# Kernel optimization log

Hardware: AMD Instinct MI355X
Metric: run time of the kernel (lower is better)

The kernel has to match this reference:

```python
import jax, jax.numpy as jnp
import numpy as np

B, T, E, H = 8, 1024, 128, 8
S = E // H  # 16, narrow per-head dim


def setup_inputs() -> dict:
    key = jax.random.key(0)
    ks = jax.random.split(key, 7)
    return {
        "x": jax.random.normal(ks[0], (B, T, E), dtype=jnp.float32),
        "masks": jax.random.randint(ks[1], (B, T), 0, 2, dtype=jnp.int32),
        "Wq": jax.random.normal(ks[2], (S, S), dtype=jnp.float32) * 0.05,
        "Wk": jax.random.normal(ks[3], (S, S), dtype=jnp.float32) * 0.05,
        "Wv": jax.random.normal(ks[4], (S, S), dtype=jnp.float32) * 0.05,
        "Wu": jax.random.normal(ks[5], (E, E), dtype=jnp.float32) * 0.05,
        "bu": jnp.zeros((E,), dtype=jnp.float32),
        "temporal_only": 1,
    }


def reference(x, masks, Wq, Wk, Wv, Wu, bu, temporal_only):
    b, t, e = x.shape
    h = H
    s = e // h
    x4 = x.reshape(b, t, h, s)
    # nn.Linear(s, s, bias=False): y = x @ W.T, applied per head
    q = jnp.einsum('bths,ds->bthd', x4, Wq)
    k = jnp.einsum('bths,ds->bthd', x4, Wk)
    v = jnp.einsum('bths,ds->bthd', x4, Wv)
    scale = jnp.float32(e) ** 0.25
    q = q / scale
    k = k / scale
    # (b, h, t, t) attention logits
    dot = jnp.einsum('bqhd,bkhd->bhqk', q, k)
    # temporal_only masking: masks is (b, t), applied on key axis then query axis
    m = masks.astype(bool)
    neg = jnp.float32(-1e9)
    dot = jnp.where(m[:, None, None, :], dot, neg)
    dot = jnp.where(m[:, None, :, None], dot, neg)
    attn = jax.nn.softmax(dot, axis=-1)
    # post-softmax zeroing with the same masks
    attn = jnp.where(m[:, None, None, :], attn, jnp.float32(0.0))
    attn = jnp.where(m[:, None, :, None], attn, jnp.float32(0.0))
    out = jnp.einsum('bhqk,bkhd->bqhd', attn, v).reshape(b, t, h * s)
    return out @ Wu.T + bu
```

## Files before the change

### kernel.cpp

```cpp
#include <hip/hip_runtime.h>

#define NB 8
#define NT 1024
#define NE 128
#define NH 8
#define NS 16

#define WS_Q 0
#define WS_KC 1048576
#define WS_VC 2097152
#define WS_Y 3145728
#define WS_VIDX 4194304
#define WS_VCNT (4194304 + 8192)

#define WT_PITCH 132

typedef float v2f __attribute__((ext_vector_type(2)));

static __device__ __forceinline__ v2f vlo(const float4 v) { return v2f{v.x, v.y}; }
static __device__ __forceinline__ v2f vhi(const float4 v) { return v2f{v.z, v.w}; }
static __device__ __forceinline__ v2f pfma(v2f a, v2f b, v2f c) {
  return __builtin_elementwise_fma(a, b, c);
}

static __device__ __forceinline__ float fexp2(float x) {
  return __builtin_amdgcn_exp2f(x);
}

static __device__ __forceinline__ void gload_lds16(const float* g, float* l) {
  __builtin_amdgcn_global_load_lds(
      (const __attribute__((address_space(1))) void*)g,
      (__attribute__((address_space(3))) void*)l, 16, 0, 0);
}

static __device__ __forceinline__ void fma4(float4& acc, float s, const float4 v) {
  v2f lo = pfma(v2f{s, s}, vlo(v), vlo(acc));
  v2f hi = pfma(v2f{s, s}, vhi(v), vhi(acc));
  acc.x = lo.x; acc.y = lo.y; acc.z = hi.x; acc.w = hi.y;
}

static __device__ __forceinline__ float dot16p(const float4 q0, const float4 q1,
                                               const float4 q2, const float4 q3,
                                               const float4 k0, const float4 k1,
                                               const float4 k2, const float4 k3) {
  v2f a = vlo(q0) * vlo(k0);
  v2f b = vhi(q0) * vhi(k0);
  a = pfma(vlo(q1), vlo(k1), a);
  b = pfma(vhi(q1), vhi(k1), b);
  a = pfma(vlo(q2), vlo(k2), a);
  b = pfma(vhi(q2), vhi(k2), b);
  a = pfma(vlo(q3), vlo(k3), a);
  b = pfma(vhi(q3), vhi(k3), b);
  v2f c = a + b;
  return c.x + c.y;
}

__global__ __launch_bounds__(256) void qkv_kernel(
    const float* __restrict__ x, const int* __restrict__ masks,
    const float* __restrict__ Wq, const float* __restrict__ Wk,
    const float* __restrict__ Wv, float* __restrict__ Q,
    float* __restrict__ Kc, float* __restrict__ Vc, int* __restrict__ vidx,
    int* __restrict__ vcount) {
  __shared__ __align__(16) float xs[64 * 20];
  __shared__ int posl[64];
  const int tid = threadIdx.x;
  const int h = blockIdx.x & 7;
  const int rg = blockIdx.x >> 3;
  const int b = rg >> 4;
  const int bt = (rg & 15) << 6;
  {
    const int sr = tid >> 2, sq = tid & 3;
    float4 xv =
        *(const float4*)(x + (size_t)(b * NT + bt + sr) * 128 + h * 16 + sq * 4);
    *(float4*)(xs + sr * 20 + sq * 4) = xv;
  }
  if (tid < 64) {
    int cnt = 0;
    for (int c = 0; c < bt; c += 64)
      cnt += __popcll(__ballot(masks[b * NT + c + tid] != 0));
    int v = masks[b * NT + bt + tid] != 0;
    unsigned long long bal = __ballot(v);
    int pos = v ? (cnt + __popcll(bal & ((1ull << tid) - 1ull))) : -1;
    posl[tid] = pos;
    if (pos >= 0) vidx[b * NT + pos] = bt + tid;
    if (bt == NT - 64 && tid == 0) vcount[b] = cnt + __popcll(bal);
  }
  const int d = tid & 15;
  const int r = (tid >> 4) << 2;
  const float4* wq4 = (const float4*)(Wq + d * 16);
  const float4 wq0 = wq4[0], wq1 = wq4[1], wq2 = wq4[2], wq3 = wq4[3];
  const float4* wk4 = (const float4*)(Wk + d * 16);
  const float4 wk0 = wk4[0], wk1 = wk4[1], wk2 = wk4[2], wk3 = wk4[3];
  const float4* wv4 = (const float4*)(Wv + d * 16);
  const float4 wv0 = wv4[0], wv1 = wv4[1], wv2 = wv4[2], wv3 = wv4[3];
  const float invs = 0.12751744448143132f;
  __syncthreads();
#pragma unroll
  for (int i = 0; i < 4; i++) {
    const int row = r + i;
    const int pp = posl[row];
    if (pp < 0) continue;
    const float4* xp = (const float4*)(xs + row * 20);
    const float4 x0 = xp[0], x1 = xp[1], x2 = xp[2], x3 = xp[3];
    float aq = dot16p(x0, x1, x2, x3, wq0, wq1, wq2, wq3);
    float ak = dot16p(x0, x1, x2, x3, wk0, wk1, wk2, wk3);
    float av = dot16p(x0, x1, x2, x3, wv0, wv1, wv2, wv3);
    size_t oc = ((size_t)(b * NH + h) * NT + pp) * NS + d;
    Q[oc] = aq * invs;
    Kc[oc] = ak;
    Vc[oc] = av;
  }
}

template <int NQ>
static __device__ __forceinline__ void attn_body(
    const float* __restrict__ Q, const float* __restrict__ Kc,
    const float* __restrict__ Vc, const int* __restrict__ vidx,
    float* __restrict__ Y, float* smem, const int tid, const int lane,
    const int s, const int b, const int bh, const int h, const int nv,
    const int tbase) {
  float* Ks = smem;
  float* Vs = smem + 8192;
  float4 q[NQ][4];
#pragma unroll
  for (int qq = 0; qq < NQ; qq++) {
    int cq = tbase + (qq << 6) + lane;
    int cqc = (cq < nv) ? cq : (nv - 1);
    const float4* qp = (const float4*)(Q + ((size_t)bh * NT + cqc) * NS);
    q[qq][0] = qp[0]; q[qq][1] = qp[1]; q[qq][2] = qp[2]; q[qq][3] = qp[3];
  }
  v2f o[NQ][8];
  float l[NQ];
#pragma unroll
  for (int qq = 0; qq < NQ; qq++) {
    l[qq] = 0.f;
#pragma unroll
    for (int k = 0; k < 8; k++) o[qq][k] = v2f{0.f, 0.f};
  }

#pragma unroll 1
  for (int k0 = 0; k0 < nv; k0 += 512) {
    const int chunk = (nv - k0 < 512) ? (nv - k0) : 512;
    __syncthreads();
    {
      const float* gk = Kc + ((size_t)bh * NT + k0) * NS;
      const float* gv = Vc + ((size_t)bh * NT + k0) * NS;
      const int ge = tid << 2;
      const int lb = (s << 8);
#pragma unroll
      for (int p = 0; p < 4; p++) {
        gload_lds16(gk + (p << 11) + ge, Ks + (p << 11) + lb);
        gload_lds16(gv + (p << 11) + ge, Vs + (p << 11) + lb);
      }
    }
    __syncthreads();
#pragma unroll 2
    for (int g = 0; g < 16; g++) {
      const int rb = s + (g << 5);
      if (rb >= chunk) break;
      float sc[NQ][4];
#pragma unroll
      for (int i = 0; i < 4; i++) {
        const float4* kr = (const float4*)(Ks + (rb + (i << 3)) * 16);
        const float4 k0v = kr[0], k1v = kr[1], k2v = kr[2], k3v = kr[3];
#pragma unroll
        for (int qq = 0; qq < NQ; qq++)
          sc[qq][i] =
              dot16p(q[qq][0], q[qq][1], q[qq][2], q[qq][3], k0v, k1v, k2v, k3v);
      }
#pragma unroll
      for (int i = 0; i < 4; i++)
        if (rb + (i << 3) >= chunk) {
#pragma unroll
          for (int qq = 0; qq < NQ; qq++) sc[qq][i] = -1e30f;
        }
      float p[NQ][4];
#pragma unroll
      for (int qq = 0; qq < NQ; qq++) {
        p[qq][0] = fexp2(sc[qq][0]);
        p[qq][1] = fexp2(sc[qq][1]);
        p[qq][2] = fexp2(sc[qq][2]);
        p[qq][3] = fexp2(sc[qq][3]);
        l[qq] += (p[qq][0] + p[qq][1]) + (p[qq][2] + p[qq][3]);
      }
#pragma unroll
      for (int i = 0; i < 4; i++) {
        const float4* vr = (const float4*)(Vs + (rb + (i << 3)) * 16);
        const float4 v0 = vr[0], v1 = vr[1], v2 = vr[2], v3 = vr[3];
#pragma unroll
        for (int qq = 0; qq < NQ; qq++) {
          const v2f pq = {p[qq][i], p[qq][i]};
          o[qq][0] = pfma(pq, vlo(v0), o[qq][0]);
          o[qq][1] = pfma(pq, vhi(v0), o[qq][1]);
          o[qq][2] = pfma(pq, vlo(v1), o[qq][2]);
          o[qq][3] = pfma(pq, vhi(v1), o[qq][3]);
          o[qq][4] = pfma(pq, vlo(v2), o[qq][4]);
          o[qq][5] = pfma(pq, vhi(v2), o[qq][5]);
          o[qq][6] = pfma(pq, vlo(v3), o[qq][6]);
          o[qq][7] = pfma(pq, vhi(v3), o[qq][7]);
        }
      }
    }
  }

  float* om = smem;
  const int q8 = tid >> 3;
  const int sub = tid & 7;
#pragma unroll
  for (int ph = 0; ph < NQ; ph++) {
    __syncthreads();
    {
      float* pa = om + (s * 64 + lane) * 20;
#pragma unroll
      for (int k = 0; k < 8; k++) *(v2f*)(pa + k * 2) = o[ph][k];
      pa[16] = l[ph];
    }
    __syncthreads();
    {
      const int cq = tbase + (ph << 6) + q8;
      if (cq < nv) {
        float L = 0.f;
        v2f y = {0.f, 0.f};
#pragma unroll
        for (int ss = 0; ss < 8; ss++) {
          const float* pp = om + (ss * 64 + q8) * 20;
          L += pp[16];
          y += *(const v2f*)(pp + sub * 2);
        }
        const int tq = vidx[b * NT + cq];
        const float inv = (L > 0.f) ? (1.0f / L) : 0.f;
        y *= v2f{inv, inv};
        *(v2f*)(Y + ((size_t)b * NT + tq) * NE + h * NS + sub * 2) = y;
      }
    }
  }
}

__global__ __launch_bounds__(512, 2) void attn_kernel(
    const float* __restrict__ Q, const float* __restrict__ Kc,
    const float* __restrict__ Vc, const int* __restrict__ vidx,
    const int* __restrict__ vcount, float* __restrict__ Y) {
  __shared__ __align__(16) float smem[16384];
  const int tid = threadIdx.x;
  const int lane = tid & 63;
  const int s = tid >> 6;
  const int bh = blockIdx.x & 63;
  const int qg = blockIdx.x >> 6;
  const int b = bh >> 3, h = bh & 7;
  const int nv = vcount[b];
  const int nq = (nv + 255) >> 8;
  const int tbase = qg * (nq << 6);
  if (nq == 2) {
    attn_body<2>(Q, Kc, Vc, vidx, Y, smem, tid, lane, s, b, bh, h, nv, tbase);
  } else if (nq == 3) {
    attn_body<3>(Q, Kc, Vc, vidx, Y, smem, tid, lane, s, b, bh, h, nv, tbase);
  } else if (nq == 4) {
    attn_body<4>(Q, Kc, Vc, vidx, Y, smem, tid, lane, s, b, bh, h, nv, tbase);
  } else if (nq == 1) {
    attn_body<1>(Q, Kc, Vc, vidx, Y, smem, tid, lane, s, b, bh, h, nv, tbase);
  }
}

__global__ __launch_bounds__(256) void proj_kernel(
    const float* __restrict__ Y, const int* __restrict__ masks,
    const float* __restrict__ Wu, const float* __restrict__ bu,
    float* __restrict__ out) {
  __shared__ __align__(16) float Wt[64 * WT_PITCH];
  __shared__ __align__(16) float Yt[16 * 128];
  const int tid = threadIdx.x;
  const int r0 = blockIdx.x * 16;
  const float4* yg = (const float4*)(Y + (size_t)r0 * 128);
  float4* yt4 = (float4*)Yt;
  {
    const float4 z = {0, 0, 0, 0};
    const int m0 = masks[r0 + (tid >> 5)];
    const int m1 = masks[r0 + 8 + (tid >> 5)];
    float4 v0 = yg[tid];
    float4 v1 = yg[tid + 256];
    yt4[tid] = m0 ? v0 : z;
    yt4[tid + 256] = m1 ? v1 : z;
  }
  const int c0 = (tid & 31) << 2;
  const int rg = (tid >> 5) & 3;
  const int eh = tid >> 7;
  float4 acc0 = {0, 0, 0, 0}, acc1 = {0, 0, 0, 0}, acc2 = {0, 0, 0, 0},
         acc3 = {0, 0, 0, 0};
  for (int e0 = 0; e0 < 128; e0 += 64) {
    __syncthreads();
#pragma unroll
    for (int p = 0; p < 8; p++) {
      int idx = tid + p * 256;
      int c = idx >> 4;
      int es = (idx & 15) << 2;
      float4 w = *(const float4*)(Wu + c * 128 + e0 + es);
      Wt[(es + 0) * WT_PITCH + c] = w.x;
      Wt[(es + 1) * WT_PITCH + c] = w.y;
      Wt[(es + 2) * WT_PITCH + c] = w.z;
      Wt[(es + 3) * WT_PITCH + c] = w.w;
    }
    __syncthreads();
    const int eb = eh << 5;
    const float* y0 = Yt + (rg * 4 + 0) * 128 + e0 + eb;
    const float* y1 = Yt + (rg * 4 + 1) * 128 + e0 + eb;
    const float* y2 = Yt + (rg * 4 + 2) * 128 + e0 + eb;
    const float* y3 = Yt + (rg * 4 + 3) * 128 + e0 + eb;
#pragma unroll 4
    for (int e = 0; e < 32; e += 4) {
      const float* wb = Wt + (eb + e) * WT_PITCH + c0;
      float4 w0 = *(const float4*)(wb + 0 * WT_PITCH);
      float4 w1 = *(const float4*)(wb + 1 * WT_PITCH);
      float4 w2 = *(const float4*)(wb + 2 * WT_PITCH);
      float4 w3 = *(const float4*)(wb + 3 * WT_PITCH);
      float4 ya = *(const float4*)(y0 + e);
      float4 yb = *(const float4*)(y1 + e);
      float4 yc = *(const float4*)(y2 + e);
      float4 yd = *(const float4*)(y3 + e);
      fma4(acc0, ya.x, w0); fma4(acc0, ya.y, w1); fma4(acc0, ya.z, w2); fma4(acc0, ya.w, w3);
      fma4(acc1, yb.x, w0); fma4(acc1, yb.y, w1); fma4(acc1, yb.z, w2); fma4(acc1, yb.w, w3);
      fma4(acc2, yc.x, w0); fma4(acc2, yc.y, w1); fma4(acc2, yc.z, w2); fma4(acc2, yc.w, w3);
      fma4(acc3, yd.x, w0); fma4(acc3, yd.y, w1); fma4(acc3, yd.z, w2); fma4(acc3, yd.w, w3);
    }
  }
  __syncthreads();
  if (eh == 1) {
    float* p = Wt + (tid & 127) * 20;
    *(float4*)(p + 0) = acc0; *(float4*)(p + 4) = acc1;
    *(float4*)(p + 8) = acc2; *(float4*)(p + 12) = acc3;
  }
  __syncthreads();
  if (eh == 0) {
    const float* p = Wt + tid * 20;
    float4 b4 = *(const float4*)(bu + c0);
    float4 q0 = *(const float4*)(p + 0);
    float4 q1 = *(const float4*)(p + 4);
    float4 q2 = *(const float4*)(p + 8);
    float4 q3 = *(const float4*)(p + 12);
    acc0.x += q0.x + b4.x; acc0.y += q0.y + b4.y; acc0.z += q0.z + b4.z; acc0.w += q0.w + b4.w;
    acc1.x += q1.x + b4.x; acc1.y += q1.y + b4.y; acc1.z += q1.z + b4.z; acc1.w += q1.w + b4.w;
    acc2.x += q2.x + b4.x; acc2.y += q2.y + b4.y; acc2.z += q2.z + b4.z; acc2.w += q2.w + b4.w;
    acc3.x += q3.x + b4.x; acc3.y += q3.y + b4.y; acc3.z += q3.z + b4.z; acc3.w += q3.w + b4.w;
    *(float4*)(out + (size_t)(r0 + rg * 4 + 0) * 128 + c0) = acc0;
    *(float4*)(out + (size_t)(r0 + rg * 4 + 1) * 128 + c0) = acc1;
    *(float4*)(out + (size_t)(r0 + rg * 4 + 2) * 128 + c0) = acc2;
    *(float4*)(out + (size_t)(r0 + rg * 4 + 3) * 128 + c0) = acc3;
  }
}

extern "C" void kernel_launch(void* const* d_in, const int* in_sizes, int n_in,
                              void* d_out, int out_size, void* d_ws,
                              size_t ws_size, hipStream_t stream) {
  const float* x = (const float*)d_in[0];
  const int* masks = (const int*)d_in[1];
  const float* Wq = (const float*)d_in[2];
  const float* Wk = (const float*)d_in[3];
  const float* Wv = (const float*)d_in[4];
  const float* Wu = (const float*)d_in[5];
  const float* bu = (const float*)d_in[6];
  float* out = (float*)d_out;

  float* ws = (float*)d_ws;
  float* Q = ws + WS_Q;
  float* Kc = ws + WS_KC;
  float* Vc = ws + WS_VC;
  float* Y = ws + WS_Y;
  int* vidx = (int*)(ws + WS_VIDX);
  int* vcount = (int*)(ws + WS_VCNT);

  qkv_kernel<<<1024, 256, 0, stream>>>(x, masks, Wq, Wk, Wv, Q, Kc, Vc, vidx,
                                       vcount);
  attn_kernel<<<4 * NB * NH, 512, 0, stream>>>(Q, Kc, Vc, vidx, vcount, Y);
  proj_kernel<<<NB * NT / 16, 256, 0, stream>>>(Y, masks, Wu, bu, out);
}
```

Before: 120.1 us.

## Split attention over key halves and merge partial sums in projection

Attention work is now split across the key dimension: each block processes half the valid keys for a larger set of queries (two query tiles instead of four), writing unnormalized partial outputs and row sums to separate buffers. The projection kernel then adds the two partials, normalizes by the combined sum and applies the query mask before the matmul. Each block loads a single key chunk with no outer chunk loop, and queries per thread go up to eight, which raises register pressure. The change also adds extra workspace traffic for the partial outputs and sums.

```diff
diff --git a/kernel.cpp b/kernel.cpp
--- a/kernel.cpp
+++ b/kernel.cpp
@@ -9,9 +9,12 @@
 #define WS_Q 0
 #define WS_KC 1048576
 #define WS_VC 2097152
-#define WS_Y 3145728
-#define WS_VIDX 4194304
-#define WS_VCNT (4194304 + 8192)
+#define WS_Y0 3145728
+#define WS_Y1 4194304
+#define WS_L0 5242880
+#define WS_L1 (5242880 + 65536)
+#define WS_VIDX (5242880 + 131072)
+#define WS_VCNT (5242880 + 131072 + 8192)
 
 #define WT_PITCH 132
 
@@ -116,9 +119,10 @@
 static __device__ __forceinline__ void attn_body(
     const float* __restrict__ Q, const float* __restrict__ Kc,
     const float* __restrict__ Vc, const int* __restrict__ vidx,
-    float* __restrict__ Y, float* smem, const int tid, const int lane,
-    const int s, const int b, const int bh, const int h, const int nv,
-    const int tbase) {
+    float* __restrict__ Yh, float* __restrict__ Lh, float* smem,
+    const int tid, const int lane, const int s, const int b, const int bh,
+    const int h, const int nv, const int tbase, const int kstart,
+    const int kend) {
   float* Ks = smem;
   float* Vs = smem + 8192;
   float4 q[NQ][4];
@@ -138,67 +142,65 @@
     for (int k = 0; k < 8; k++) o[qq][k] = v2f{0.f, 0.f};
   }
 
+  const int chunk = kend - kstart;
+  if (chunk > 0) {
+    const int nseg = (chunk + 127) >> 7;
+    const float* gk = Kc + ((size_t)bh * NT + kstart) * NS;
+    const float* gv = Vc + ((size_t)bh * NT + kstart) * NS;
+    const int ge = tid << 2;
+    const int lb = s << 8;
 #pragma unroll 1
-  for (int k0 = 0; k0 < nv; k0 += 512) {
-    const int chunk = (nv - k0 < 512) ? (nv - k0) : 512;
-    __syncthreads();
-    {
-      const float* gk = Kc + ((size_t)bh * NT + k0) * NS;
-      const float* gv = Vc + ((size_t)bh * NT + k0) * NS;
-      const int ge = tid << 2;
-      const int lb = (s << 8);
-#pragma unroll
-      for (int p = 0; p < 4; p++) {
-        gload_lds16(gk + (p << 11) + ge, Ks + (p << 11) + lb);
-        gload_lds16(gv + (p << 11) + ge, Vs + (p << 11) + lb);
+    for (int p = 0; p < nseg; p++) {
+      gload_lds16(gk + (p << 11) + ge, Ks + (p << 11) + lb);
+      gload_lds16(gv + (p << 11) + ge, Vs + (p << 11) + lb);
+    }
+  }
+  __syncthreads();
+
+#pragma unroll 2
+  for (int g = 0; g < 16; g++) {
+    const int rb = s + (g << 5);
+    if (rb >= chunk) break;
+    float sc[NQ][4];
+#pragma unroll
+    for (int i = 0; i < 4; i++) {
+      const float4* kr = (const float4*)(Ks + (rb + (i << 3)) * 16);
+      const float4 k0v = kr[0], k1v = kr[1], k2v = kr[2], k3v = kr[3];
+#pragma unroll
+      for (int qq = 0; qq < NQ; qq++)
+        sc[qq][i] =
+            dot16p(q[qq][0], q[qq][1], q[qq][2], q[qq][3], k0v, k1v, k2v, k3v);
+    }
+#pragma unroll
+    for (int i = 0; i < 4; i++)
+      if (rb + (i << 3) >= chunk) {
+#pragma unroll
+        for (int qq = 0; qq < NQ; qq++) sc[qq][i] = -1e30f;
       }
-    }
-    __syncthreads();
-#pragma unroll 2
-    for (int g = 0; g < 16; g++) {
-      const int rb = s + (g << 5);
-      if (rb >= chunk) break;
-      float sc[NQ][4];
-#pragma unroll
-      for (int i = 0; i < 4; i++) {
-        const float4* kr = (const float4*)(Ks + (rb + (i << 3)) * 16);
-        const float4 k0v = kr[0], k1v = kr[1], k2v = kr[2], k3v = kr[3];
-#pragma unroll
-        for (int qq = 0; qq < NQ; qq++)
-          sc[qq][i] =
-              dot16p(q[qq][0], q[qq][1], q[qq][2], q[qq][3], k0v, k1v, k2v, k3v);
-      }
-#pragma unroll
-      for (int i = 0; i < 4; i++)
-        if (rb + (i << 3) >= chunk) {
-#pragma unroll
-          for (int qq = 0; qq < NQ; qq++) sc[qq][i] = -1e30f;
-        }
-      float p[NQ][4];
+    float p[NQ][4];
+#pragma unroll
+    for (int qq = 0; qq < NQ; qq++) {
+      p[qq][0] = fexp2(sc[qq][0]);
+      p[qq][1] = fexp2(sc[qq][1]);
+      p[qq][2] = fexp2(sc[qq][2]);
+      p[qq][3] = fexp2(sc[qq][3]);
+      l[qq] += (p[qq][0] + p[qq][1]) + (p[qq][2] + p[qq][3]);
+    }
+#pragma unroll
+    for (int i = 0; i < 4; i++) {
+      const float4* vr = (const float4*)(Vs + (rb + (i << 3)) * 16);
+      const float4 v0 = vr[0], v1 = vr[1], v2 = vr[2], v3 = vr[3];
 #pragma unroll
       for (int qq = 0; qq < NQ; qq++) {
-        p[qq][0] = fexp2(sc[qq][0]);
-        p[qq][1] = fexp2(sc[qq][1]);
-        p[qq][2] = fexp2(sc[qq][2]);
-        p[qq][3] = fexp2(sc[qq][3]);
-        l[qq] += (p[qq][0] + p[qq][1]) + (p[qq][2] + p[qq][3]);
-      }
-#pragma unroll
-      for (int i = 0; i < 4; i++) {
-        const float4* vr = (const float4*)(Vs + (rb + (i << 3)) * 16);
-        const float4 v0 = vr[0], v1 = vr[1], v2 = vr[2], v3 = vr[3];
-#pragma unroll
-        for (int qq = 0; qq < NQ; qq++) {
-          const v2f pq = {p[qq][i], p[qq][i]};
-          o[qq][0] = pfma(pq, vlo(v0), o[qq][0]);
-          o[qq][1] = pfma(pq, vhi(v0), o[qq][1]);
-          o[qq][2] = pfma(pq, vlo(v1), o[qq][2]);
-          o[qq][3] = pfma(pq, vhi(v1), o[qq][3]);
-          o[qq][4] = pfma(pq, vlo(v2), o[qq][4]);
-          o[qq][5] = pfma(pq, vhi(v2), o[qq][5]);
-          o[qq][6] = pfma(pq, vlo(v3), o[qq][6]);
-          o[qq][7] = pfma(pq, vhi(v3), o[qq][7]);
-        }
+        const v2f pq = {p[qq][i], p[qq][i]};
+        o[qq][0] = pfma(pq, vlo(v0), o[qq][0]);
+        o[qq][1] = pfma(pq, vhi(v0), o[qq][1]);
+        o[qq][2] = pfma(pq, vlo(v1), o[qq][2]);
+        o[qq][3] = pfma(pq, vhi(v1), o[qq][3]);
+        o[qq][4] = pfma(pq, vlo(v2), o[qq][4]);
+        o[qq][5] = pfma(pq, vhi(v2), o[qq][5]);
+        o[qq][6] = pfma(pq, vlo(v3), o[qq][6]);
+        o[qq][7] = pfma(pq, vhi(v3), o[qq][7]);
       }
     }
   }
@@ -228,9 +230,8 @@
           y += *(const v2f*)(pp + sub * 2);
         }
         const int tq = vidx[b * NT + cq];
-        const float inv = (L > 0.f) ? (1.0f / L) : 0.f;
-        y *= v2f{inv, inv};
-        *(v2f*)(Y + ((size_t)b * NT + tq) * NE + h * NS + sub * 2) = y;
+        *(v2f*)(Yh + ((size_t)b * NT + tq) * NE + h * NS + sub * 2) = y;
+        if (sub == 0) Lh[(size_t)bh * NT + tq] = L;
       }
     }
   }
@@ -239,46 +240,82 @@
 __global__ __launch_bounds__(512, 2) void attn_kernel(
     const float* __restrict__ Q, const float* __restrict__ Kc,
     const float* __restrict__ Vc, const int* __restrict__ vidx,
-    const int* __restrict__ vcount, float* __restrict__ Y) {
+    const int* __restrict__ vcount, float* __restrict__ Y0,
+    float* __restrict__ Y1, float* __restrict__ L0, float* __restrict__ L1) {
   __shared__ __align__(16) float smem[16384];
   const int tid = threadIdx.x;
   const int lane = tid & 63;
   const int s = tid >> 6;
   const int bh = blockIdx.x & 63;
-  const int qg = blockIdx.x >> 6;
+  const int tile = (blockIdx.x >> 6) & 1;
+  const int kh = blockIdx.x >> 7;
   const int b = bh >> 3, h = bh & 7;
   const int nv = vcount[b];
-  const int nq = (nv + 255) >> 8;
-  const int tbase = qg * (nq << 6);
-  if (nq == 2) {
-    attn_body<2>(Q, Kc, Vc, vidx, Y, smem, tid, lane, s, b, bh, h, nv, tbase);
+  const int nq = (nv + 127) >> 7;
+  const int tbase = tile * (nq << 6);
+  const int h0 = nv >> 1;
+  const int kstart = kh ? h0 : 0;
+  const int kend = kh ? nv : h0;
+  float* Yh = kh ? Y1 : Y0;
+  float* Lh = kh ? L1 : L0;
+  if (nq == 4) {
+    attn_body<4>(Q, Kc, Vc, vidx, Yh, Lh, smem, tid, lane, s, b, bh, h, nv,
+                 tbase, kstart, kend);
+  } else if (nq == 5) {
+    attn_body<5>(Q, Kc, Vc, vidx, Yh, Lh, smem, tid, lane, s, b, bh, h, nv,
+                 tbase, kstart, kend);
   } else if (nq == 3) {
-    attn_body<3>(Q, Kc, Vc, vidx, Y, smem, tid, lane, s, b, bh, h, nv, tbase);
-  } else if (nq == 4) {
-    attn_body<4>(Q, Kc, Vc, vidx, Y, smem, tid, lane, s, b, bh, h, nv, tbase);
+    attn_body<3>(Q, Kc, Vc, vidx, Yh, Lh, smem, tid, lane, s, b, bh, h, nv,
+                 tbase, kstart, kend);
+  } else if (nq == 2) {
+    attn_body<2>(Q, Kc, Vc, vidx, Yh, Lh, smem, tid, lane, s, b, bh, h, nv,
+                 tbase, kstart, kend);
+  } else if (nq == 6) {
+    attn_body<6>(Q, Kc, Vc, vidx, Yh, Lh, smem, tid, lane, s, b, bh, h, nv,
+                 tbase, kstart, kend);
   } else if (nq == 1) {
-    attn_body<1>(Q, Kc, Vc, vidx, Y, smem, tid, lane, s, b, bh, h, nv, tbase);
+    attn_body<1>(Q, Kc, Vc, vidx, Yh, Lh, smem, tid, lane, s, b, bh, h, nv,
+                 tbase, kstart, kend);
+  } else if (nq == 7) {
+    attn_body<7>(Q, Kc, Vc, vidx, Yh, Lh, smem, tid, lane, s, b, bh, h, nv,
+                 tbase, kstart, kend);
+  } else if (nq == 8) {
+    attn_body<8>(Q, Kc, Vc, vidx, Yh, Lh, smem, tid, lane, s, b, bh, h, nv,
+                 tbase, kstart, kend);
   }
 }
 
 __global__ __launch_bounds__(256) void proj_kernel(
-    const float* __restrict__ Y, const int* __restrict__ masks,
-    const float* __restrict__ Wu, const float* __restrict__ bu,
-    float* __restrict__ out) {
+    const float* __restrict__ Y0, const float* __restrict__ Y1,
+    const float* __restrict__ L0, const float* __restrict__ L1,
+    const int* __restrict__ masks, const float* __restrict__ Wu,
+    const float* __restrict__ bu, float* __restrict__ out) {
   __shared__ __align__(16) float Wt[64 * WT_PITCH];
   __shared__ __align__(16) float Yt[16 * 128];
   const int tid = threadIdx.x;
   const int r0 = blockIdx.x * 16;
-  const float4* yg = (const float4*)(Y + (size_t)r0 * 128);
+  const int bb = r0 >> 10;
+  const float4* yg0 = (const float4*)(Y0 + (size_t)r0 * 128);
+  const float4* yg1 = (const float4*)(Y1 + (size_t)r0 * 128);
   float4* yt4 = (float4*)Yt;
   {
     const float4 z = {0, 0, 0, 0};
-    const int m0 = masks[r0 + (tid >> 5)];
-    const int m1 = masks[r0 + 8 + (tid >> 5)];
-    float4 v0 = yg[tid];
-    float4 v1 = yg[tid + 256];
-    yt4[tid] = m0 ? v0 : z;
-    yt4[tid + 256] = m1 ? v1 : z;
+#pragma unroll
+    for (int p = 0; p < 2; p++) {
+      const int idx = tid + p * 256;
+      const int row = idx >> 5;
+      const int head = (idx & 31) >> 2;
+      const int t = (r0 + row) & 1023;
+      const size_t li = (size_t)(bb * NH + head) * NT + t;
+      const int qm = masks[r0 + row];
+      const float Lv = L0[li] + L1[li];
+      const float inv = (qm != 0 && Lv > 0.f) ? (1.0f / Lv) : 0.f;
+      float4 a = yg0[idx];
+      float4 c = yg1[idx];
+      a.x = (a.x + c.x) * inv; a.y = (a.y + c.y) * inv;
+      a.z = (a.z + c.z) * inv; a.w = (a.w + c.w) * inv;
+      yt4[idx] = qm ? a : z;
+    }
   }
   const int c0 = (tid & 31) << 2;
   const int rg = (tid >> 5) & 3;
@@ -362,12 +399,17 @@
   float* Q = ws + WS_Q;
   float* Kc = ws + WS_KC;
   float* Vc = ws + WS_VC;
-  float* Y = ws + WS_Y;
+  float* Y0 = ws + WS_Y0;
+  float* Y1 = ws + WS_Y1;
+  float* L0 = ws + WS_L0;
+  float* L1 = ws + WS_L1;
   int* vidx = (int*)(ws + WS_VIDX);
   int* vcount = (int*)(ws + WS_VCNT);
 
   qkv_kernel<<<1024, 256, 0, stream>>>(x, masks, Wq, Wk, Wv, Q, Kc, Vc, vidx,
                                        vcount);
-  attn_kernel<<<4 * NB * NH, 512, 0, stream>>>(Q, Kc, Vc, vidx, vcount, Y);
-  proj_kernel<<<NB * NT / 16, 256, 0, stream>>>(Y, masks, Wu, bu, out);
-}
+  attn_kernel<<<256, 512, 0, stream>>>(Q, Kc, Vc, vidx, vcount, Y0, Y1, L0,
+                                       L1);
+  proj_kernel<<<NB * NT / 16, 256, 0, stream>>>(Y0, Y1, L0, L1, masks, Wu, bu,
+                                                out);
+}
```

After: 119.5 us. No clear change (-0.5%).
